# Kernel optimization log

Hardware: AMD Instinct MI355X
Metric: run time of the kernel (lower is better)

## Reference

```python
import jax, jax.numpy as jnp
import numpy as np

N_NODES = 50000
N_EDGES = 800000
NODE_F = 64
HID = 64
LSTM_F = 32
LSTM_H = 128
B = 64
T = 200
OUT = 1
N_LAYERS = 2


def setup_inputs() -> dict:
    key = jax.random.key(0)
    ks = jax.random.split(key, 16)
    s = 0.05
    return {
        "x": jax.random.normal(ks[0], (N_NODES, NODE_F), jnp.float32),
        "edge_attr": jax.random.normal(ks[1], (N_EDGES, NODE_F), jnp.float32),
        "x_seq": jax.random.normal(ks[2], (B, T, LSTM_F), jnp.float32),
        "lin_W": jax.random.normal(ks[3], (N_LAYERS, HID, HID), jnp.float32) * s,
        "lin_b": jnp.zeros((N_LAYERS, HID), jnp.float32),
        "mlp_W1": jax.random.normal(ks[4], (N_LAYERS, HID, HID), jnp.float32) * s,
        "mlp_b1": jnp.zeros((N_LAYERS, HID), jnp.float32),
        "mlp_W2": jax.random.normal(ks[5], (N_LAYERS, HID, HID), jnp.float32) * s,
        "mlp_b2": jnp.zeros((N_LAYERS, HID), jnp.float32),
        "eps": jnp.zeros((N_LAYERS,), jnp.float32),
        "ln_scale": jnp.ones((N_LAYERS, HID), jnp.float32),
        "ln_bias": jnp.zeros((N_LAYERS, HID), jnp.float32),
        "W_ih": jax.random.normal(ks[6], (4 * LSTM_H, HID + LSTM_F), jnp.float32) * s,
        "W_hh": jax.random.normal(ks[7], (4 * LSTM_H, LSTM_H), jnp.float32) * s,
        "b_ih": jnp.zeros((4 * LSTM_H,), jnp.float32),
        "b_hh": jnp.zeros((4 * LSTM_H,), jnp.float32),
        "lstm_ln_scale": jnp.ones((LSTM_H,), jnp.float32),
        "lstm_ln_bias": jnp.zeros((LSTM_H,), jnp.float32),
        "fc_W": jax.random.normal(ks[8], (OUT, LSTM_H), jnp.float32) * s,
        "fc_b": jnp.zeros((OUT,), jnp.float32),
        "edge_index": jax.random.randint(ks[9], (2, N_EDGES), 0, N_NODES, jnp.int32),
        "node_indices": jax.random.randint(ks[10], (B,), 0, N_NODES, jnp.int32),
    }


def _layernorm(z, scale, bias, eps=1e-5):
    mu = jnp.mean(z, axis=-1, keepdims=True)
    var = jnp.var(z, axis=-1, keepdims=True)
    return (z - mu) * jax.lax.rsqrt(var + eps) * scale + bias


def reference(x, edge_attr, x_seq, lin_W, lin_b, mlp_W1, mlp_b1, mlp_W2, mlp_b2,
              eps, ln_scale, ln_bias, W_ih, W_hh, b_ih, b_hh,
              lstm_ln_scale, lstm_ln_bias, fc_W, fc_b, edge_index, node_indices):
    src, dst = edge_index[0], edge_index[1]
    h = x
    n = x.shape[0]
    # GINEConv layers: out = MLP((1+eps)*x + sum_j relu(x_j + lin(e_ij)))
    for l in range(N_LAYERS):
        e = edge_attr @ lin_W[l].T + lin_b[l]            # [E, C]
        m = jax.nn.relu(h[src] + e)                       # gather + message
        agg = jax.ops.segment_sum(m, dst, num_segments=n) # scatter-add
        z = (1.0 + eps[l]) * h + agg
        z = jax.nn.relu(z @ mlp_W1[l].T + mlp_b1[l]) @ mlp_W2[l].T + mlp_b2[l]
        z = _layernorm(z, ln_scale[l], ln_bias[l])
        h = jax.nn.relu(z)

    sel = h[node_indices]                                 # [B, HID]
    seq_len = x_seq.shape[1]
    expanded = jnp.broadcast_to(sel[:, None, :], (sel.shape[0], seq_len, sel.shape[1]))
    combined = jnp.concatenate([expanded, x_seq], axis=2) # [B, T, HID+F]

    # single-layer LSTM, PyTorch gate order (i, f, g, o)
    Hd = W_hh.shape[1]
    xs = jnp.transpose(combined, (1, 0, 2))               # [T, B, D]
    x_proj = xs @ W_ih.T + b_ih                            # [T, B, 4H]

    def step(carry, xp):
        hprev, cprev = carry
        gates = xp + hprev @ W_hh.T + b_hh
        i, f, g, o = jnp.split(gates, 4, axis=-1)
        i = jax.nn.sigmoid(i); f = jax.nn.sigmoid(f)
        g = jnp.tanh(g); o = jax.nn.sigmoid(o)
        c = f * cprev + i * g
        hn = o * jnp.tanh(c)
        return (hn, c), None

    bsz = combined.shape[0]
    init = (jnp.zeros((bsz, Hd), combined.dtype), jnp.zeros((bsz, Hd), combined.dtype))
    (hn, _), _ = jax.lax.scan(step, init, x_proj)

    last = _layernorm(hn, lstm_ln_scale, lstm_ln_bias)
    return last @ fc_W.T + fc_b
```

## Files before the change

### kernel.cpp

```cpp
#include <hip/hip_runtime.h>
#include <cmath>

static constexpr int NN  = 50000;
static constexpr int NE  = 800000;
static constexpr int HID = 64;
static constexpr int BB  = 64;
static constexpr int TT  = 200;
static constexpr int LH  = 128;
static constexpr int G4  = 512;

static constexpr int SCB = 125;
static constexpr int SCH = 400;

typedef _Float16 h2 __attribute__((ext_vector_type(2)));

#ifndef __has_builtin
#define __has_builtin(x) 0
#endif
#if __has_builtin(__builtin_amdgcn_fdot2)
__device__ __forceinline__ float fdot2_(h2 a, h2 b, float c) {
    return __builtin_amdgcn_fdot2(a, b, c, false);
}
#else
__device__ __forceinline__ float fdot2_(h2 a, h2 b, float c) {
    return c + (float)a.x * (float)b.x + (float)a.y * (float)b.y;
}
#endif

__device__ __forceinline__ h2 as_h2(unsigned int u) {
    union { unsigned int u; h2 h; } cv; cv.u = u; return cv.h;
}

__device__ __forceinline__ float sigmoid_fast(float x) {
    return __fdividef(1.f, 1.f + __expf(-x));
}
__device__ __forceinline__ float tanh_fast(float x) {
    return __fdividef(2.f, 1.f + __expf(-2.f * x)) - 1.f;
}

__global__ __launch_bounds__(256) void hist_kernel(const int* __restrict__ dsts,
                                                   int* __restrict__ deg) {
    int i = blockIdx.x * 256 + threadIdx.x;
    if (i < NE) atomicAdd(&deg[dsts[i]], 1);
}

__global__ __launch_bounds__(512) void scan1_kernel(const int* __restrict__ deg,
                                                    int* __restrict__ loc,
                                                    int* __restrict__ bsum) {
    __shared__ int ws[8];
    const int b = blockIdx.x, t = threadIdx.x;
    const int idx = b * SCH + t;
    const int lane = t & 63, wv = t >> 6;
    int v = (t < SCH && idx < NN) ? deg[idx] : 0;
    int x = v;
    #pragma unroll
    for (int off = 1; off < 64; off <<= 1) {
        int y = __shfl_up(x, off);
        if (lane >= off) x += y;
    }
    if (lane == 63) ws[wv] = x;
    __syncthreads();
    if (t < 8) {
        int s = ws[t];
        #pragma unroll
        for (int off = 1; off < 8; off <<= 1) {
            int y = __shfl_up(s, off);
            if (t >= off) s += y;
        }
        ws[t] = s;
    }
    __syncthreads();
    const int base = wv ? ws[wv - 1] : 0;
    if (t < SCH && idx < NN) loc[idx] = base + x - v;
    if (t == 511) bsum[b] = ws[7];
}

__global__ void scan2_kernel(const int* __restrict__ bsum,
                             int* __restrict__ boff,
                             int* __restrict__ rowptr) {
    int tot = 0;
    for (int i = 0; i < SCB; ++i) { boff[i] = tot; tot += bsum[i]; }
    rowptr[NN] = tot;
}

__global__ __launch_bounds__(512) void scan3_kernel(const int* __restrict__ loc,
                                                    const int* __restrict__ boff,
                                                    int* __restrict__ rowptr,
                                                    int* __restrict__ head) {
    const int b = blockIdx.x, t = threadIdx.x;
    const int idx = b * SCH + t;
    if (t < SCH && idx < NN) {
        int r = loc[idx] + boff[b];
        rowptr[idx] = r;
        head[idx] = r;
    }
}

__global__ __launch_bounds__(256) void scatter_kernel(const int* __restrict__ srcs,
                                                      const int* __restrict__ dsts,
                                                      int* __restrict__ head,
                                                      int* __restrict__ perm,
                                                      int* __restrict__ ssrc) {
    int e = blockIdx.x * 256 + threadIdx.x;
    if (e < NE) {
        int d = dsts[e];
        int pos = atomicAdd(&head[d], 1);
        perm[e] = pos;
        ssrc[pos] = srcs[e];
    }
}

__global__ __launch_bounds__(256) void permute_kernel(const float* __restrict__ ea,
                                                      const int* __restrict__ perm,
                                                      ushort4* __restrict__ easort) {
    const int lane = threadIdx.x & 63, wid = threadIdx.x >> 6;
    const int slot = lane >> 4, hw = lane & 15;
    const int e = (blockIdx.x * 4 + wid) * 4 + slot;
    if (e < NE) {
        const int p = perm[e];
        float4 v = ((const float4*)ea)[(size_t)e * 16 + hw];
        union { _Float16 h[4]; ushort4 u; } pk;
        pk.h[0] = (_Float16)v.x; pk.h[1] = (_Float16)v.y;
        pk.h[2] = (_Float16)v.z; pk.h[3] = (_Float16)v.w;
        easort[(size_t)p * 16 + hw] = pk.u;
    }
}

__global__ __launch_bounds__(256) void edge_agg_kernel(
    const float*   __restrict__ h_in,
    const ushort4* __restrict__ easort,
    const float*   __restrict__ W,
    const float*   __restrict__ bias,
    const int*     __restrict__ rowptr,
    const int*     __restrict__ ssrc,
    float*         __restrict__ agg)
{
    __shared__ ushort4 stage[4][64];
    const int lane = threadIdx.x & 63;
    const int wid  = threadIdx.x >> 6;
    const int slot = lane >> 4, hw = lane & 15;

    h2 w2[32];
    {
        const float4* wf = (const float4*)(W + lane * 64);
        #pragma unroll
        for (int k4 = 0; k4 < 16; ++k4) {
            float4 v = wf[k4];
            h2 a; a.x = (_Float16)v.x; a.y = (_Float16)v.y;
            h2 b; b.x = (_Float16)v.z; b.y = (_Float16)v.w;
            w2[2*k4] = a; w2[2*k4+1] = b;
        }
    }
    const float bc = bias[lane];

    const int gw = blockIdx.x * 4 + wid;
    const int nw = gridDim.x * 4;
    for (int n = gw; n < NN; n += nw) {
        const int ofs = rowptr[n];
        const int dg  = rowptr[n + 1] - ofs;
        float acc = 0.f;
        for (int c = 0; c < dg; c += 4) {
            const int rem = dg - c;
            const int pick = slot < rem ? slot : rem - 1;
            const int ssv = ssrc[ofs + c + pick];
            stage[wid][lane] = easort[(size_t)(ofs + c + pick) * 16 + hw];
            if (rem >= 4) {
                float hv[4];
                #pragma unroll
                for (int j = 0; j < 4; ++j) {
                    int sj = __shfl(ssv, j << 4);
                    hv[j] = h_in[(size_t)sj * HID + lane];
                }
                asm volatile("s_waitcnt lgkmcnt(0)" ::: "memory");
                #pragma unroll
                for (int j = 0; j < 4; ++j) {
                    const uint4* stu = (const uint4*)&stage[wid][j * 16];
                    float aE = bc;
                    #pragma unroll
                    for (int k = 0; k < 8; ++k) {
                        uint4 u = stu[k];
                        aE = fdot2_(as_h2(u.x), w2[4*k+0], aE);
                        aE = fdot2_(as_h2(u.y), w2[4*k+1], aE);
                        aE = fdot2_(as_h2(u.z), w2[4*k+2], aE);
                        aE = fdot2_(as_h2(u.w), w2[4*k+3], aE);
                    }
                    float m = aE + hv[j];
                    acc += m > 0.f ? m : 0.f;
                }
            } else {
                asm volatile("s_waitcnt lgkmcnt(0)" ::: "memory");
                for (int j = 0; j < rem; ++j) {
                    int sj = __shfl(ssv, j << 4);
                    const uint4* stu = (const uint4*)&stage[wid][j * 16];
                    float aE = bc;
                    #pragma unroll
                    for (int k = 0; k < 8; ++k) {
                        uint4 u = stu[k];
                        aE = fdot2_(as_h2(u.x), w2[4*k+0], aE);
                        aE = fdot2_(as_h2(u.y), w2[4*k+1], aE);
                        aE = fdot2_(as_h2(u.z), w2[4*k+2], aE);
                        aE = fdot2_(as_h2(u.w), w2[4*k+3], aE);
                    }
                    float m = aE + h_in[(size_t)sj * HID + lane];
                    acc += m > 0.f ? m : 0.f;
                }
            }
        }
        agg[(size_t)n * HID + lane] = acc;
    }
}

__global__ __launch_bounds__(256) void node_kernel(
    const float* __restrict__ h_in,
    const float* __restrict__ agg,
    const float* __restrict__ W1, const float* __restrict__ b1,
    const float* __restrict__ W2, const float* __restrict__ b2,
    const float* __restrict__ epsp,
    const float* __restrict__ lnS, const float* __restrict__ lnB,
    float*       __restrict__ h_out)
{
    __shared__ float zbuf[4][64];
    __shared__ float tbuf[4][64];
    const int lane = threadIdx.x & 63;
    const int wid  = threadIdx.x >> 6;

    float w1[64], w2[64];
    {
        const float4* wf1 = (const float4*)(W1 + lane * 64);
        const float4* wf2 = (const float4*)(W2 + lane * 64);
        #pragma unroll
        for (int k4 = 0; k4 < 16; ++k4) {
            float4 a = wf1[k4], b = wf2[k4];
            w1[4*k4+0]=a.x; w1[4*k4+1]=a.y; w1[4*k4+2]=a.z; w1[4*k4+3]=a.w;
            w2[4*k4+0]=b.x; w2[4*k4+1]=b.y; w2[4*k4+2]=b.z; w2[4*k4+3]=b.w;
        }
    }
    const float b1c = b1[lane], b2c = b2[lane];
    const float sC = lnS[lane], bC = lnB[lane];
    const float epv = 1.f + epsp[0];

    const int gw = blockIdx.x * 4 + wid;
    const int nw = gridDim.x * 4;
    for (int n = gw; n < NN; n += nw) {
        float z = epv * h_in[(size_t)n*HID + lane] + agg[(size_t)n*HID + lane];
        zbuf[wid][lane] = z;
        asm volatile("s_waitcnt lgkmcnt(0)" ::: "memory");
        float acc = b1c;
        {
            const float4* zf = (const float4*)&zbuf[wid][0];
            #pragma unroll
            for (int k4 = 0; k4 < 16; ++k4) {
                float4 v = zf[k4];
                acc = fmaf(v.x, w1[4*k4+0], acc);
                acc = fmaf(v.y, w1[4*k4+1], acc);
                acc = fmaf(v.z, w1[4*k4+2], acc);
                acc = fmaf(v.w, w1[4*k4+3], acc);
            }
        }
        acc = acc > 0.f ? acc : 0.f;
        tbuf[wid][lane] = acc;
        asm volatile("s_waitcnt lgkmcnt(0)" ::: "memory");
        float acc2 = b2c;
        {
            const float4* tf = (const float4*)&tbuf[wid][0];
            #pragma unroll
            for (int k4 = 0; k4 < 16; ++k4) {
                float4 v = tf[k4];
                acc2 = fmaf(v.x, w2[4*k4+0], acc2);
                acc2 = fmaf(v.y, w2[4*k4+1], acc2);
                acc2 = fmaf(v.z, w2[4*k4+2], acc2);
                acc2 = fmaf(v.w, w2[4*k4+3], acc2);
            }
        }
        float s1 = acc2, s2 = acc2 * acc2;
        #pragma unroll
        for (int off = 32; off >= 1; off >>= 1) {
            s1 += __shfl_xor(s1, off);
            s2 += __shfl_xor(s2, off);
        }
        float mu  = s1 * (1.f/64.f);
        float var = s2 * (1.f/64.f) - mu * mu;
        float r   = rsqrtf(var + 1e-5f);
        float o   = (acc2 - mu) * r * sC + bC;
        h_out[(size_t)n*HID + lane] = o > 0.f ? o : 0.f;
    }
}

__global__ __launch_bounds__(512) void prep_kernel(
    const float* __restrict__ Wih,
    const float* __restrict__ bih,
    const float* __restrict__ h2v,
    const int*   __restrict__ nidx,
    float*       __restrict__ W2T,
    float*       __restrict__ selp)
{
    const int g = threadIdx.x;
    if (blockIdx.x == BB) {
        #pragma unroll
        for (int k = 0; k < 32; ++k)
            W2T[k * G4 + g] = Wih[g * 96 + 64 + k];
    } else {
        const int b = blockIdx.x;
        __shared__ float hrow[64];
        if (g < 64) hrow[g] = h2v[(size_t)nidx[b] * HID + g];
        __syncthreads();
        float acc = bih[g];
        #pragma unroll
        for (int k = 0; k < 64; ++k)
            acc = fmaf(hrow[k], Wih[g * 96 + k], acc);
        selp[b * G4 + g] = acc;
    }
}

__global__ __launch_bounds__(512) void xp_kernel(
    const float* __restrict__ xseq,
    const float* __restrict__ selp,
    const float* __restrict__ W2T,
    float*       __restrict__ xp)
{
    const int g   = threadIdx.x;
    const int row = blockIdx.x;
    const int t   = row >> 6;
    const int b   = row & 63;
    __shared__ float xs[32];
    if (g < 32) xs[g] = xseq[((size_t)b * TT + t) * 32 + g];
    __syncthreads();
    float acc = selp[b * G4 + g];
    #pragma unroll
    for (int k = 0; k < 32; ++k)
        acc = fmaf(xs[k], W2T[k * G4 + g], acc);
    xp[(size_t)row * G4 + g] = acc;
}

__global__ __launch_bounds__(512) void lstm_kernel(
    const float* __restrict__ xp,
    const float* __restrict__ Whh,
    const float* __restrict__ bhh,
    const float* __restrict__ lnS, const float* __restrict__ lnB,
    const float* __restrict__ fcW,
    const float* __restrict__ fcb,
    float*       __restrict__ out)
{
    const int g = threadIdx.x;
    const int b = blockIdx.x;
    const int j = g & 127;
    const int gt = g >> 7;

    float w[128];
    {
        const float4* wf = (const float4*)(Whh + (size_t)g * LH);
        #pragma unroll
        for (int k4 = 0; k4 < 32; ++k4) {
            float4 v = wf[k4];
            w[4*k4+0]=v.x; w[4*k4+1]=v.y; w[4*k4+2]=v.z; w[4*k4+3]=v.w;
        }
    }
    const float bg = bhh[g];

    __shared__ float h_lds[LH];
    __shared__ float gates[G4];
    if (g < LH) h_lds[g] = 0.f;
    float c = 0.f;
    __syncthreads();

    float xv = xp[(size_t)b * G4 + g];

    for (int t = 0; t < TT; ++t) {
        const int tn = (t + 1 < TT) ? t + 1 : t;
        const float xv_next = xp[((size_t)tn * BB + b) * G4 + g];

        float a0 = 0.f, a1 = 0.f, a2 = 0.f, a3 = 0.f;
        const float4* h4 = (const float4*)h_lds;
        #pragma unroll
        for (int k4 = 0; k4 < 32; k4 += 4) {
            float4 v0 = h4[k4+0], v1 = h4[k4+1], v2 = h4[k4+2], v3 = h4[k4+3];
            a0 = fmaf(v0.x, w[4*k4+ 0], a0); a0 = fmaf(v0.y, w[4*k4+ 1], a0);
            a0 = fmaf(v0.z, w[4*k4+ 2], a0); a0 = fmaf(v0.w, w[4*k4+ 3], a0);
            a1 = fmaf(v1.x, w[4*k4+ 4], a1); a1 = fmaf(v1.y, w[4*k4+ 5], a1);
            a1 = fmaf(v1.z, w[4*k4+ 6], a1); a1 = fmaf(v1.w, w[4*k4+ 7], a1);
            a2 = fmaf(v2.x, w[4*k4+ 8], a2); a2 = fmaf(v2.y, w[4*k4+ 9], a2);
            a2 = fmaf(v2.z, w[4*k4+10], a2); a2 = fmaf(v2.w, w[4*k4+11], a2);
            a3 = fmaf(v3.x, w[4*k4+12], a3); a3 = fmaf(v3.y, w[4*k4+13], a3);
            a3 = fmaf(v3.z, w[4*k4+14], a3); a3 = fmaf(v3.w, w[4*k4+15], a3);
        }
        float acc = xv + bg + ((a0 + a1) + (a2 + a3));

        float act = (gt == 2) ? tanh_fast(acc) : sigmoid_fast(acc);
        gates[g] = act;
        __syncthreads();

        float iv = gates[j];
        float fv = gates[j + LH];
        float gv = gates[j + 2*LH];
        float ov = gates[j + 3*LH];
        c = fmaf(fv, c, iv * gv);
        float hv = ov * tanh_fast(c);
        if (g < LH) h_lds[j] = hv;
        __syncthreads();

        xv = xv_next;
    }

    if (g < 64) {
        float h0 = h_lds[g], h1 = h_lds[g + 64];
        float s1 = h0 + h1, s2 = h0*h0 + h1*h1;
        #pragma unroll
        for (int off = 32; off >= 1; off >>= 1) {
            s1 += __shfl_xor(s1, off);
            s2 += __shfl_xor(s2, off);
        }
        float mu  = s1 * (1.f/128.f);
        float var = s2 * (1.f/128.f) - mu * mu;
        float r   = rsqrtf(var + 1e-5f);
        float p = ((h0 - mu)*r*lnS[g]      + lnB[g])      * fcW[g]
                + ((h1 - mu)*r*lnS[g + 64] + lnB[g + 64]) * fcW[g + 64];
        #pragma unroll
        for (int off = 32; off >= 1; off >>= 1) p += __shfl_xor(p, off);
        if (g == 0) out[b] = p + fcb[0];
    }
}

extern "C" void kernel_launch(void* const* d_in, const int* in_sizes, int n_in,
                              void* d_out, int out_size, void* d_ws, size_t ws_size,
                              hipStream_t stream) {
    const float* x     = (const float*)d_in[0];
    const float* ea    = (const float*)d_in[1];
    const float* xseq  = (const float*)d_in[2];
    const float* linW  = (const float*)d_in[3];
    const float* linB  = (const float*)d_in[4];
    const float* mW1   = (const float*)d_in[5];
    const float* mb1   = (const float*)d_in[6];
    const float* mW2   = (const float*)d_in[7];
    const float* mb2   = (const float*)d_in[8];
    const float* eps   = (const float*)d_in[9];
    const float* lnS   = (const float*)d_in[10];
    const float* lnB   = (const float*)d_in[11];
    const float* Wih   = (const float*)d_in[12];
    const float* Whh   = (const float*)d_in[13];
    const float* bih   = (const float*)d_in[14];
    const float* bhh   = (const float*)d_in[15];
    const float* llnS  = (const float*)d_in[16];
    const float* llnB  = (const float*)d_in[17];
    const float* fcW   = (const float*)d_in[18];
    const float* fcb   = (const float*)d_in[19];
    const int*   eidx  = (const int*)d_in[20];
    const int*   nidx  = (const int*)d_in[21];
    float* out = (float*)d_out;

    const int* srcs = eidx;
    const int* dsts = eidx + NE;

    float* ws   = (float*)d_ws;
    float* agg  = ws;
    float* h1   = agg  + (size_t)NN * HID;
    float* h2   = h1   + (size_t)NN * HID;
    float* selp = h2   + (size_t)NN * HID;
    float* W2T  = selp + (size_t)BB * G4;
    float* xp   = W2T  + (size_t)32 * G4;
    int*   deg    = (int*)(xp + (size_t)TT * BB * G4);
    int*   rowptr = deg + NN;
    int*   head   = rowptr + NN + 2;
    int*   loc    = head + NN;
    int*   bsum   = loc + NN;
    int*   boff   = bsum + SCB + 3;
    int*   perm   = boff + SCB + 3;
    int*   ssrc   = perm + NE;
    uintptr_t ep = (uintptr_t)(ssrc + NE);
    ep = (ep + 15) & ~(uintptr_t)15;
    ushort4* easort = (ushort4*)ep;

    hipMemsetAsync(deg, 0, (size_t)NN * sizeof(int), stream);
    hist_kernel<<<(NE + 255) / 256, 256, 0, stream>>>(dsts, deg);
    scan1_kernel<<<SCB, 512, 0, stream>>>(deg, loc, bsum);
    scan2_kernel<<<1, 1, 0, stream>>>(bsum, boff, rowptr);
    scan3_kernel<<<SCB, 512, 0, stream>>>(loc, boff, rowptr, head);
    scatter_kernel<<<(NE + 255) / 256, 256, 0, stream>>>(srcs, dsts, head, perm, ssrc);
    permute_kernel<<<NE / 16, 256, 0, stream>>>(ea, perm, easort);

    edge_agg_kernel<<<2048, 256, 0, stream>>>(x, easort, linW, linB, rowptr, ssrc, agg);
    node_kernel<<<512, 256, 0, stream>>>(x, agg, mW1, mb1, mW2, mb2, eps, lnS, lnB, h1);
    edge_agg_kernel<<<2048, 256, 0, stream>>>(h1, easort, linW + 64*64, linB + 64, rowptr, ssrc, agg);
    node_kernel<<<512, 256, 0, stream>>>(h1, agg, mW1 + 64*64, mb1 + 64, mW2 + 64*64, mb2 + 64,
                                         eps + 1, lnS + 64, lnB + 64, h2);
    prep_kernel<<<BB + 1, 512, 0, stream>>>(Wih, bih, h2, nidx, W2T, selp);
    xp_kernel<<<TT * BB, 512, 0, stream>>>(xseq, selp, W2T, xp);
    lstm_kernel<<<BB, 512, 0, stream>>>(xp, Whh, bhh, llnS, llnB, fcW, fcb, out);
}
```

Baseline: 678.2 us.

## Interleave LSTM gates per lane, exchange via shuffles, fp16 dot recurrence

Reorders the gate layout so the four gates of each hidden unit sit in adjacent lanes. Gate values are exchanged with warp shuffles instead of a shared-memory round trip, which removes one barrier per timestep, and h is double-buffered in LDS. The recurrent weights and h are stored as fp16 pairs and accumulated with fdot2, halving register and LDS traffic. The risk is precision loss in the 200-step recurrence from fp16 weights and hidden state.

```diff
diff --git a/kernel.cpp b/kernel.cpp
--- a/kernel.cpp
+++ b/kernel.cpp
@@ -29,6 +29,9 @@
 
 __device__ __forceinline__ h2 as_h2(unsigned int u) {
     union { unsigned int u; h2 h; } cv; cv.u = u; return cv.h;
+}
+__device__ __forceinline__ unsigned int as_u32(h2 h) {
+    union { h2 h; unsigned int u; } cv; cv.h = h; return cv.u;
 }
 
 __device__ __forceinline__ float sigmoid_fast(float x) {
@@ -295,10 +298,11 @@
     float*       __restrict__ selp)
 {
     const int g = threadIdx.x;
+    const int pos = ((g & 127) << 2) | (g >> 7);
     if (blockIdx.x == BB) {
         #pragma unroll
         for (int k = 0; k < 32; ++k)
-            W2T[k * G4 + g] = Wih[g * 96 + 64 + k];
+            W2T[k * G4 + pos] = Wih[g * 96 + 64 + k];
     } else {
         const int b = blockIdx.x;
         __shared__ float hrow[64];
@@ -308,7 +312,7 @@
         #pragma unroll
         for (int k = 0; k < 64; ++k)
             acc = fmaf(hrow[k], Wih[g * 96 + k], acc);
-        selp[b * G4 + g] = acc;
+        selp[b * G4 + pos] = acc;
     }
 }
 
@@ -341,68 +345,97 @@
     const float* __restrict__ fcb,
     float*       __restrict__ out)
 {
-    const int g = threadIdx.x;
-    const int b = blockIdx.x;
-    const int j = g & 127;
-    const int gt = g >> 7;
-
-    float w[128];
+    const int t  = threadIdx.x;
+    const int b  = blockIdx.x;
+    const int gt = t & 3;
+    const int j  = t >> 2;
+    const int gate = gt * LH + j;
+
+    h2 w2[64];
     {
-        const float4* wf = (const float4*)(Whh + (size_t)g * LH);
+        const float4* wf = (const float4*)(Whh + (size_t)gate * LH);
         #pragma unroll
         for (int k4 = 0; k4 < 32; ++k4) {
             float4 v = wf[k4];
-            w[4*k4+0]=v.x; w[4*k4+1]=v.y; w[4*k4+2]=v.z; w[4*k4+3]=v.w;
-        }
-    }
-    const float bg = bhh[g];
-
-    __shared__ float h_lds[LH];
-    __shared__ float gates[G4];
-    if (g < LH) h_lds[g] = 0.f;
+            h2 a; a.x = (_Float16)v.x; a.y = (_Float16)v.y;
+            h2 c2; c2.x = (_Float16)v.z; c2.y = (_Float16)v.w;
+            w2[2*k4] = a; w2[2*k4+1] = c2;
+        }
+    }
+    const float bg = bhh[gate];
+    const float s_ = (gt == 2) ? 2.f : 1.f;
+    const float a_ = (gt == 2) ? 2.f : 1.f;
+    const float d_ = (gt == 2) ? -1.f : 0.f;
+
+    __shared__ unsigned int h2b0[64];
+    __shared__ unsigned int h2b1[64];
+    __shared__ float h_final[LH];
+    if (t < 64) h2b0[t] = 0u;
     float c = 0.f;
     __syncthreads();
 
-    float xv = xp[(size_t)b * G4 + g];
-
-    for (int t = 0; t < TT; ++t) {
-        const int tn = (t + 1 < TT) ? t + 1 : t;
-        const float xv_next = xp[((size_t)tn * BB + b) * G4 + g];
+    float xv = xp[(size_t)b * G4 + t];
+
+    auto step = [&](const unsigned int* hb, unsigned int* hw, int ts) {
+        const int tn = (ts + 1 < TT) ? ts + 1 : ts;
+        const float xv_next = xp[((size_t)tn * BB + b) * G4 + t];
 
         float a0 = 0.f, a1 = 0.f, a2 = 0.f, a3 = 0.f;
-        const float4* h4 = (const float4*)h_lds;
-        #pragma unroll
-        for (int k4 = 0; k4 < 32; k4 += 4) {
-            float4 v0 = h4[k4+0], v1 = h4[k4+1], v2 = h4[k4+2], v3 = h4[k4+3];
-            a0 = fmaf(v0.x, w[4*k4+ 0], a0); a0 = fmaf(v0.y, w[4*k4+ 1], a0);
-            a0 = fmaf(v0.z, w[4*k4+ 2], a0); a0 = fmaf(v0.w, w[4*k4+ 3], a0);
-            a1 = fmaf(v1.x, w[4*k4+ 4], a1); a1 = fmaf(v1.y, w[4*k4+ 5], a1);
-            a1 = fmaf(v1.z, w[4*k4+ 6], a1); a1 = fmaf(v1.w, w[4*k4+ 7], a1);
-            a2 = fmaf(v2.x, w[4*k4+ 8], a2); a2 = fmaf(v2.y, w[4*k4+ 9], a2);
-            a2 = fmaf(v2.z, w[4*k4+10], a2); a2 = fmaf(v2.w, w[4*k4+11], a2);
-            a3 = fmaf(v3.x, w[4*k4+12], a3); a3 = fmaf(v3.y, w[4*k4+13], a3);
-            a3 = fmaf(v3.z, w[4*k4+14], a3); a3 = fmaf(v3.w, w[4*k4+15], a3);
+        const uint4* hb4 = (const uint4*)hb;
+        #pragma unroll
+        for (int k = 0; k < 16; k += 4) {
+            uint4 u0 = hb4[k], u1 = hb4[k+1], u2 = hb4[k+2], u3 = hb4[k+3];
+            a0 = fdot2_(as_h2(u0.x), w2[4*k+ 0], a0);
+            a0 = fdot2_(as_h2(u0.y), w2[4*k+ 1], a0);
+            a0 = fdot2_(as_h2(u0.z), w2[4*k+ 2], a0);
+            a0 = fdot2_(as_h2(u0.w), w2[4*k+ 3], a0);
+            a1 = fdot2_(as_h2(u1.x), w2[4*k+ 4], a1);
+            a1 = fdot2_(as_h2(u1.y), w2[4*k+ 5], a1);
+            a1 = fdot2_(as_h2(u1.z), w2[4*k+ 6], a1);
+            a1 = fdot2_(as_h2(u1.w), w2[4*k+ 7], a1);
+            a2 = fdot2_(as_h2(u2.x), w2[4*k+ 8], a2);
+            a2 = fdot2_(as_h2(u2.y), w2[4*k+ 9], a2);
+            a2 = fdot2_(as_h2(u2.z), w2[4*k+10], a2);
+            a2 = fdot2_(as_h2(u2.w), w2[4*k+11], a2);
+            a3 = fdot2_(as_h2(u3.x), w2[4*k+12], a3);
+            a3 = fdot2_(as_h2(u3.y), w2[4*k+13], a3);
+            a3 = fdot2_(as_h2(u3.z), w2[4*k+14], a3);
+            a3 = fdot2_(as_h2(u3.w), w2[4*k+15], a3);
         }
         float acc = xv + bg + ((a0 + a1) + (a2 + a3));
 
-        float act = (gt == 2) ? tanh_fast(acc) : sigmoid_fast(acc);
-        gates[g] = act;
+        float act = fmaf(a_, __fdividef(1.f, 1.f + __expf(-s_ * acc)), d_);
+
+        float v0 = act;
+        float v1 = __shfl_xor(v0, 1);
+        float v2 = __shfl_xor(v0, 2);
+        float v3 = __shfl_xor(v1, 2);
+        float iv = (gt==0)?v0:(gt==1)?v1:(gt==2)?v2:v3;
+        float fv = (gt==1)?v0:(gt==0)?v1:(gt==3)?v2:v3;
+        float gv = (gt==2)?v0:(gt==3)?v1:(gt==0)?v2:v3;
+        float ov = (gt==3)?v0:(gt==2)?v1:(gt==1)?v2:v3;
+
+        c = fmaf(fv, c, iv * gv);
+        float hval = ov * tanh_fast(c);
+
+        float hpart = __shfl_xor(hval, 4);
+        if ((t & 7) == 0) {
+            h2 p; p.x = (_Float16)hval; p.y = (_Float16)hpart;
+            hw[j >> 1] = as_u32(p);
+        }
+        if (gt == 0) h_final[j] = hval;
         __syncthreads();
 
-        float iv = gates[j];
-        float fv = gates[j + LH];
-        float gv = gates[j + 2*LH];
-        float ov = gates[j + 3*LH];
-        c = fmaf(fv, c, iv * gv);
-        float hv = ov * tanh_fast(c);
-        if (g < LH) h_lds[j] = hv;
-        __syncthreads();
-
         xv = xv_next;
-    }
-
-    if (g < 64) {
-        float h0 = h_lds[g], h1 = h_lds[g + 64];
+    };
+
+    for (int ts = 0; ts < TT; ts += 2) {
+        step(h2b0, h2b1, ts);
+        step(h2b1, h2b0, ts + 1);
+    }
+
+    if (t < 64) {
+        float h0 = h_final[t], h1 = h_final[t + 64];
         float s1 = h0 + h1, s2 = h0*h0 + h1*h1;
         #pragma unroll
         for (int off = 32; off >= 1; off >>= 1) {
@@ -412,11 +445,11 @@
         float mu  = s1 * (1.f/128.f);
         float var = s2 * (1.f/128.f) - mu * mu;
         float r   = rsqrtf(var + 1e-5f);
-        float p = ((h0 - mu)*r*lnS[g]      + lnB[g])      * fcW[g]
-                + ((h1 - mu)*r*lnS[g + 64] + lnB[g + 64]) * fcW[g + 64];
+        float p = ((h0 - mu)*r*lnS[t]      + lnB[t])      * fcW[t]
+                + ((h1 - mu)*r*lnS[t + 64] + lnB[t + 64]) * fcW[t + 64];
         #pragma unroll
         for (int off = 32; off >= 1; off >>= 1) p += __shfl_xor(p, off);
-        if (g == 0) out[b] = p + fcb[0];
+        if (t == 0) out[b] = p + fcb[0];
     }
 }
 
@@ -453,8 +486,8 @@
     float* ws   = (float*)d_ws;
     float* agg  = ws;
     float* h1   = agg  + (size_t)NN * HID;
-    float* h2   = h1   + (size_t)NN * HID;
-    float* selp = h2   + (size_t)NN * HID;
+    float* h2m  = h1   + (size_t)NN * HID;
+    float* selp = h2m  + (size_t)NN * HID;
     float* W2T  = selp + (size_t)BB * G4;
     float* xp   = W2T  + (size_t)32 * G4;
     int*   deg    = (int*)(xp + (size_t)TT * BB * G4);
@@ -481,8 +514,8 @@
     node_kernel<<<512, 256, 0, stream>>>(x, agg, mW1, mb1, mW2, mb2, eps, lnS, lnB, h1);
     edge_agg_kernel<<<2048, 256, 0, stream>>>(h1, easort, linW + 64*64, linB + 64, rowptr, ssrc, agg);
     node_kernel<<<512, 256, 0, stream>>>(h1, agg, mW1 + 64*64, mb1 + 64, mW2 + 64*64, mb2 + 64,
-                                         eps + 1, lnS + 64, lnB + 64, h2);
-    prep_kernel<<<BB + 1, 512, 0, stream>>>(Wih, bih, h2, nidx, W2T, selp);
+                                         eps + 1, lnS + 64, lnB + 64, h2m);
+    prep_kernel<<<BB + 1, 512, 0, stream>>>(Wih, bih, h2m, nidx, W2T, selp);
     xp_kernel<<<TT * BB, 512, 0, stream>>>(xseq, selp, W2T, xp);
     lstm_kernel<<<BB, 512, 0, stream>>>(xp, Whh, bhh, llnS, llnB, fcW, fcb, out);
 }
```

Result: no change. 665.6 us (-1.9%).
